# Kernel tuning notes

Measured on AMD Instinct MI355X. Metric: run time of the kernel, lower is better.

## Reference

```python
import jax, jax.numpy as jnp
import numpy as np

# db4 analysis filters (pywt convention); synthesis reuses same filters (orthogonal wavelet,
# correlation analysis + convolution synthesis gives perfect reconstruction under periodization).
DEC_LO = [-0.010597401784997278, 0.032883011666982945, 0.030841381835986965, -0.18703481171888114,
          -0.02798376941698385, 0.6308807679295904, 0.7148465705525415, 0.23037781330885523]
DEC_HI = [-0.23037781330885523, 0.7148465705525415, -0.6308807679295904, -0.02798376941698385,
          0.18703481171888114, 0.030841381835986965, -0.032883011666982945, -0.010597401784997278]
LEVELS = 3

def _analysis(x, filt):
    # a[n] = sum_k filt[k] * x[(2n+k) mod L]  (circular filter + downsample-by-2)
    y = sum(c * jnp.roll(x, -k, axis=-1) for k, c in enumerate(filt))
    return y[..., ::2]

def _synthesis(a, filt):
    # upsample-by-2 (zeros at odd positions) then circular convolution with filt
    u = jnp.zeros(a.shape[:-1] + (2 * a.shape[-1],), a.dtype).at[..., ::2].set(a)
    return sum(c * jnp.roll(u, k, axis=-1) for k, c in enumerate(filt))

def _decompose(z, levels):
    details, cur = [], z
    for _ in range(levels):
        details.append(_analysis(cur, DEC_HI))
        cur = _analysis(cur, DEC_LO)
    return cur, details

def _reconstruct(approx, details):
    cur = approx
    for d in reversed(details):
        cur = _synthesis(cur, DEC_LO) + _synthesis(d, DEC_HI)
    return cur

def _soft_threshold(c, lam_raw):
    # dynamic per-(batch,channel) threshold scaled by learnable softplus(lam_raw)
    lam = jax.nn.softplus(lam_raw) * jnp.mean(jnp.abs(c), axis=-1)  # [B,H]
    thr = jnp.sign(c) * jnp.maximum(jnp.abs(c) - lam[..., None], 0.0)
    return thr, lam

def _film(c, flow_raw, Wgb, bgb, Wg, bg):
    # FiLM gamma/beta from flow features, sigmoid-gated
    gb = flow_raw @ Wgb.T + bgb                      # [B, 2H]
    H = c.shape[1]
    gamma, beta = gb[:, :H], gb[:, H:]
    gate = jax.nn.sigmoid(flow_raw @ Wg + bg)[:, None, None]  # [B,1,1]
    return c * (1.0 + gate * gamma[:, :, None]) + gate * beta[:, :, None]

def setup_inputs() -> dict:
    key = jax.random.key(0)
    ks = jax.random.split(key, 8)
    B, L, C, Hd = 16, 4096, 64, 128
    x = jax.random.normal(ks[0], (B, L, C), jnp.float32)
    mask = jnp.ones((B, L), jnp.float32)
    flow_raw = jax.random.normal(ks[1], (B, 24), jnp.float32)
    W_in = jax.random.normal(ks[2], (Hd, C), jnp.float32) / np.sqrt(C)
    b_in = jnp.zeros((Hd,), jnp.float32)
    W_mix = jax.random.normal(ks[3], (Hd, Hd), jnp.float32) / np.sqrt(Hd)
    b_mix = jnp.zeros((Hd,), jnp.float32)
    lam_raw = jnp.full((LEVELS + 1,), 0.5413248538970947, jnp.float32)  # softplus^-1(1.0)
    film_Wgb = jax.random.normal(ks[4], (LEVELS + 1, 2 * Hd, 24), jnp.float32) * 0.05
    film_bgb = jnp.zeros((LEVELS + 1, 2 * Hd), jnp.float32)
    film_Wg = jax.random.normal(ks[5], (LEVELS + 1, 24), jnp.float32) * 0.05
    film_bg = jnp.zeros((LEVELS + 1,), jnp.float32)
    return dict(x=x, mask=mask, flow_raw=flow_raw, W_in=W_in, b_in=b_in, W_mix=W_mix, b_mix=b_mix,
                lam_raw=lam_raw, film_Wgb=film_Wgb, film_bgb=film_bgb, film_Wg=film_Wg, film_bg=film_bg)

def reference(x, mask, flow_raw, W_in, b_in, W_mix, b_mix, lam_raw, film_Wgb, film_bgb, film_Wg, film_bg):
    xp = x.transpose(0, 2, 1) * mask[:, None, :]               # [B,C,L]
    z = jnp.einsum('hc,bcl->bhl', W_in, xp) + b_in[:, None]    # input_proj (1x1 conv)
    approx, details = _decompose(z, LEVELS)
    approx = _film(approx, flow_raw, film_Wgb[0], film_bgb[0], film_Wg[0], film_bg[0])
    details = [_film(d, flow_raw, film_Wgb[i + 1], film_bgb[i + 1], film_Wg[i + 1], film_bg[i + 1])
               for i, d in enumerate(details)]
    approx_t, lam_a = _soft_threshold(approx, lam_raw[0])
    dts, lams = [], [lam_a]
    for i, d in enumerate(details):
        dt, lam_d = _soft_threshold(d, lam_raw[i + 1])
        dts.append(dt)
        lams.append(lam_d)
    z_rec = _reconstruct(approx_t, dts)
    mixed = jnp.einsum('gh,bhl->bgl', W_mix, z + z_rec) + b_mix[:, None]  # mix (1x1 conv)
    out = jax.nn.gelu(mixed, approximate=False)                 # torch nn.GELU is exact
    h_seq = out.transpose(0, 2, 1) * mask[..., None]            # [B,L,H]
    denom = jnp.clip(jnp.sum(mask, axis=1, keepdims=True), 1.0, None)
    h_pool = jnp.sum(h_seq * mask[..., None], axis=1) / denom   # masked mean pool [B,H]
    lam_cat = jnp.concatenate([l.reshape(l.shape[0], -1) for l in lams], axis=1)
    return h_seq, h_pool, jnp.mean(lam_cat, axis=1), jnp.max(lam_cat, axis=1)
```

## Files before the change

kernel.cpp:

```cpp
#include <hip/hip_runtime.h>
#include <math.h>

#define BB 16
#define LL 4096
#define CC 64
#define HD 128

typedef __attribute__((ext_vector_type(8))) short short8;
typedef __attribute__((ext_vector_type(8))) unsigned short ushort8;
typedef __attribute__((ext_vector_type(4))) float floatx4;

__constant__ float c_lo[8] = {
    -0.010597401784997278f, 0.032883011666982945f, 0.030841381835986965f,
    -0.18703481171888114f, -0.02798376941698385f, 0.6308807679295904f,
    0.7148465705525415f, 0.23037781330885523f};
__constant__ float c_hi[8] = {
    -0.23037781330885523f, 0.7148465705525415f, -0.6308807679295904f,
    -0.02798376941698385f, 0.18703481171888114f, 0.030841381835986965f,
    -0.032883011666982945f, -0.010597401784997278f};

__device__ __forceinline__ float gelu_fast(float x) {
    float u = x * fmaf(0.044715f * x, x, 1.0f) * 1.5957691216057308f;
    return x / (1.0f + __expf(-u));
}
__device__ __forceinline__ unsigned short f2b(float f) {
    unsigned int u = __float_as_uint(f);
    u = u + 0x7FFFu + ((u >> 16) & 1u);
    return (unsigned short)(u >> 16);
}
__device__ __forceinline__ float b2f(unsigned short s) {
    return __uint_as_float(((unsigned int)s) << 16);
}


__global__ __launch_bounds__(256) void zproj_kernel(
    const float* __restrict__ x, const float* __restrict__ mask,
    const float* __restrict__ W_in, const float* __restrict__ b_in,
    unsigned short* __restrict__ z_bf,
    const float* __restrict__ W_mix, unsigned short* __restrict__ Bmix,
    const float* __restrict__ flow, const float* __restrict__ Wgb,
    const float* __restrict__ bgb, const float* __restrict__ Wg,
    const float* __restrict__ bg, float* __restrict__ film_ws,
    float* __restrict__ gate_ws) {
    int blk = blockIdx.x;
    int tid = threadIdx.x;

    if (blk >= BB * 64) {
        int e = blk - BB * 64;
        if (e < 64) {
            int q = e * 256 + tid;
            int g = (q >> 3) & 127;
            int h = ((q >> 10) << 3) | (q & 7);
            Bmix[q] = f2b(W_mix[g * HD + h]);
        } else {
            int bf = e - 64;
            int f = bf & 3;
            int b = bf >> 2;
            const float* fl = flow + b * 24;
            const float* wrow = Wgb + ((size_t)(f * 256 + tid)) * 24;
            float acc = bgb[f * 256 + tid];
#pragma unroll
            for (int j = 0; j < 24; ++j) acc = fmaf(wrow[j], fl[j], acc);
            film_ws[(size_t)bf * 256 + tid] = acc;
            if (tid == 0) {
                float g = bg[f];
#pragma unroll
                for (int j = 0; j < 24; ++j) g = fmaf(Wg[f * 24 + j], fl[j], g);
                gate_ws[bf] = 1.0f / (1.0f + expf(-g));
            }
        }
        return;
    }

    int b = blk >> 6;
    int l0 = (blk & 63) << 6;
    int lane = tid & 63;
    int w = tid >> 6;
    int h_half = w >> 1;
    int l_q = w & 1;
    int ln15 = lane & 15, lq4 = lane >> 4;

    int lr0 = l0 + l_q * 32 + ln15;
    int lr1 = lr0 + 16;
    float mk0 = mask[(size_t)b * LL + lr0];
    float mk1 = mask[(size_t)b * LL + lr1];

    floatx4 acc[4][2];
#pragma unroll
    for (int i = 0; i < 4; ++i)
#pragma unroll
        for (int j = 0; j < 2; ++j) acc[i][j] = (floatx4){0.f, 0.f, 0.f, 0.f};

#pragma unroll
    for (int ks = 0; ks < 2; ++ks) {
        int c0 = ks * 32 + (lq4 << 3);
        short8 bf0, bf1;
        {
            const float* xp = x + ((size_t)b * LL + lr0) * CC + c0;
            float4 xa = *(const float4*)xp;
            float4 xb = *(const float4*)(xp + 4);
            bf0[0] = (short)f2b(xa.x * mk0); bf0[1] = (short)f2b(xa.y * mk0);
            bf0[2] = (short)f2b(xa.z * mk0); bf0[3] = (short)f2b(xa.w * mk0);
            bf0[4] = (short)f2b(xb.x * mk0); bf0[5] = (short)f2b(xb.y * mk0);
            bf0[6] = (short)f2b(xb.z * mk0); bf0[7] = (short)f2b(xb.w * mk0);
        }
        {
            const float* xp = x + ((size_t)b * LL + lr1) * CC + c0;
            float4 xa = *(const float4*)xp;
            float4 xb = *(const float4*)(xp + 4);
            bf1[0] = (short)f2b(xa.x * mk1); bf1[1] = (short)f2b(xa.y * mk1);
            bf1[2] = (short)f2b(xa.z * mk1); bf1[3] = (short)f2b(xa.w * mk1);
            bf1[4] = (short)f2b(xb.x * mk1); bf1[5] = (short)f2b(xb.y * mk1);
            bf1[6] = (short)f2b(xb.z * mk1); bf1[7] = (short)f2b(xb.w * mk1);
        }
        const float* wb = W_in + (size_t)(h_half * 64 + ln15) * CC + c0;
#pragma unroll
        for (int ht = 0; ht < 4; ++ht) {
            const float* wr = wb + (size_t)ht * 16 * CC;
            float4 wa = *(const float4*)wr;
            float4 wc = *(const float4*)(wr + 4);
            short8 af;
            af[0] = (short)f2b(wa.x); af[1] = (short)f2b(wa.y);
            af[2] = (short)f2b(wa.z); af[3] = (short)f2b(wa.w);
            af[4] = (short)f2b(wc.x); af[5] = (short)f2b(wc.y);
            af[6] = (short)f2b(wc.z); af[7] = (short)f2b(wc.w);
            acc[ht][0] = __builtin_amdgcn_mfma_f32_16x16x32_bf16(bf0, af, acc[ht][0], 0, 0, 0);
            acc[ht][1] = __builtin_amdgcn_mfma_f32_16x16x32_bf16(bf1, af, acc[ht][1], 0, 0, 0);
        }
    }

#pragma unroll
    for (int ht = 0; ht < 4; ++ht) {
        int h = h_half * 64 + ht * 16 + ln15;
        float bi = b_in[h];
        unsigned short* zr = z_bf + ((size_t)(b * HD + h)) * LL;
#pragma unroll
        for (int j = 0; j < 2; ++j) {
            int lbase = l0 + l_q * 32 + j * 16 + (lq4 << 2);
            ushort4 o;
            o.x = f2b(acc[ht][j][0] + bi);
            o.y = f2b(acc[ht][j][1] + bi);
            o.z = f2b(acc[ht][j][2] + bi);
            o.w = f2b(acc[ht][j][3] + bi);
            *(ushort4*)(zr + lbase) = o;
        }
    }
}


__device__ __forceinline__ void analysis_step(const float* __restrict__ src,
                                              float* __restrict__ lo_dst,
                                              float* __restrict__ hi_dst,
                                              int half, int tid) {
    int len = half << 1;
    for (int q = tid; q < (half >> 2); q += 256) {
        int n0 = q << 2;
        float lo[4], hi[4];
        if (n0 + 4 == half) {
#pragma unroll
            for (int i = 0; i < 4; ++i) {
                float l = 0.f, hh = 0.f;
#pragma unroll
                for (int k = 0; k < 8; ++k) {
                    float v = src[(2 * (n0 + i) + k) & (len - 1)];
                    l = fmaf(c_lo[k], v, l);
                    hh = fmaf(c_hi[k], v, hh);
                }
                lo[i] = l; hi[i] = hh;
            }
        } else {
            float sv[16];
            const float* sp = src + (n0 << 1);
            *(float4*)&sv[0]  = *(const float4*)(sp);
            *(float4*)&sv[4]  = *(const float4*)(sp + 4);
            *(float4*)&sv[8]  = *(const float4*)(sp + 8);
            *(float4*)&sv[12] = *(const float4*)(sp + 12);
#pragma unroll
            for (int i = 0; i < 4; ++i) {
                float l = 0.f, hh = 0.f;
#pragma unroll
                for (int k = 0; k < 8; ++k) {
                    l = fmaf(c_lo[k], sv[2 * i + k], l);
                    hh = fmaf(c_hi[k], sv[2 * i + k], hh);
                }
                lo[i] = l; hi[i] = hh;
            }
        }
        *(float4*)&lo_dst[n0] = make_float4(lo[0], lo[1], lo[2], lo[3]);
        *(float4*)&hi_dst[n0] = make_float4(hi[0], hi[1], hi[2], hi[3]);
    }
}

__device__ __forceinline__ void synth_oct(const float* __restrict__ A,
                                          const float* __restrict__ D,
                                          int m0, int half, float* ov) {
    if (m0 == 0) {
        int mask2 = (half << 1) - 1;
#pragma unroll
        for (int t = 0; t < 8; ++t) {
            int par = t & 1;
            float s = 0.f;
#pragma unroll
            for (int j = 0; j < 4; ++j) {
                int k = 2 * j + par;
                int idx = ((t - k) & mask2) >> 1;
                s = fmaf(c_lo[k], A[idx], s);
                s = fmaf(c_hi[k], D[idx], s);
            }
            ov[t] = s;
        }
    } else {
        float av[8], dv[8];
        *(float4*)&av[0] = *(const float4*)(A + m0 - 4);
        *(float4*)&av[4] = *(const float4*)(A + m0);
        *(float4*)&dv[0] = *(const float4*)(D + m0 - 4);
        *(float4*)&dv[4] = *(const float4*)(D + m0);
#pragma unroll
        for (int t = 0; t < 4; ++t) {
            float e = 0.f, o = 0.f;
#pragma unroll
            for (int j = 0; j < 4; ++j) {
                float xa = av[t + 4 - j], xd = dv[t + 4 - j];
                e = fmaf(c_lo[2 * j], xa, e);     e = fmaf(c_hi[2 * j], xd, e);
                o = fmaf(c_lo[2 * j + 1], xa, o); o = fmaf(c_hi[2 * j + 1], xd, o);
            }
            ov[2 * t] = e;
            ov[2 * t + 1] = o;
        }
    }
}

__device__ __forceinline__ void synth_step(const float* __restrict__ A,
                                           const float* __restrict__ D,
                                           float* __restrict__ dst,
                                           int half, int tid) {
    for (int q = tid; q < (half >> 2); q += 256) {
        int m0 = q << 2;
        int i0 = m0 << 1;
        float ov[8];
        synth_oct(A, D, m0, half, ov);
        *(float4*)&dst[i0]     = make_float4(ov[0], ov[1], ov[2], ov[3]);
        *(float4*)&dst[i0 + 4] = make_float4(ov[4], ov[5], ov[6], ov[7]);
    }
}


__global__ __launch_bounds__(256) void wavelet_kernel(const unsigned short* __restrict__ z_bf,
                                                      unsigned short* __restrict__ s_bf,
                                                      const float* __restrict__ film_ws,
                                                      const float* __restrict__ gate_ws,
                                                      const float* __restrict__ lam_raw,
                                                      float* __restrict__ lam_ws) {
    __shared__ float d1[2048];
    __shared__ float d2[1024];
    __shared__ float Aq[2048];
    __shared__ float Bq[1024];

    int blk = blockIdx.x;
    int b = blk >> 7;
    int h = blk & 127;
    int tid = threadIdx.x;
    const unsigned short* zg = z_bf + ((size_t)(b * HD + h)) * LL;
    unsigned short* sg = s_bf + ((size_t)(b * HD + h)) * LL;

    for (int q = tid; q < 512; q += 256) {
        int n0 = q << 2;
        float sv[16];
        if (n0 == 2044) {
#pragma unroll
            for (int j = 0; j < 14; ++j)
                sv[j] = b2f(zg[(2 * n0 + j) & 4095]);
            sv[14] = 0.f; sv[15] = 0.f;
        } else {
            ushort8 va = *(const ushort8*)(zg + (n0 << 1));
            ushort8 vb = *(const ushort8*)(zg + (n0 << 1) + 8);
#pragma unroll
            for (int j = 0; j < 8; ++j) {
                sv[j]     = b2f(va[j]);
                sv[8 + j] = b2f(vb[j]);
            }
        }
        float lo[4], hi[4];
#pragma unroll
        for (int i = 0; i < 4; ++i) {
            float l = 0.f, hh = 0.f;
#pragma unroll
            for (int k = 0; k < 8; ++k) {
                l = fmaf(c_lo[k], sv[2 * i + k], l);
                hh = fmaf(c_hi[k], sv[2 * i + k], hh);
            }
            lo[i] = l; hi[i] = hh;
        }
        *(float4*)&Aq[n0] = make_float4(lo[0], lo[1], lo[2], lo[3]);
        *(float4*)&d1[n0] = make_float4(hi[0], hi[1], hi[2], hi[3]);
    }
    __syncthreads();
    analysis_step(Aq, Bq, d2, 1024, tid);
    __syncthreads();
    analysis_step(Bq, Aq, Aq + 512, 512, tid);
    __syncthreads();

    float sc0, sh0, sc1, sh1, sc2, sh2, sc3, sh3;
    {
        int base = b * 4;
#define FILM_COEF(bd, SC, SH)                                              \
        {   float ga = film_ws[((size_t)(base + bd)) * 256 + h];           \
            float be = film_ws[((size_t)(base + bd)) * 256 + 128 + h];     \
            float gt = gate_ws[base + bd];                                 \
            SC = 1.0f + gt * ga; SH = gt * be; }
        FILM_COEF(0, sc0, sh0) FILM_COEF(1, sc1, sh1)
        FILM_COEF(2, sc2, sh2) FILM_COEF(3, sc3, sh3)
#undef FILM_COEF
    }

    float* p0 = &Aq[tid << 2];
    float* p1 = &d1[tid << 2];
    float* p2 = &d1[1024 + (tid << 2)];
    float* p3 = &d2[tid << 2];
    bool lowhalf = (tid < 128);
    float scA = lowhalf ? sc0 : sc3, shA = lowhalf ? sh0 : sh3;

    float4 f0 = *(float4*)p0, f1 = *(float4*)p1, f2v = *(float4*)p2, f3 = *(float4*)p3;
#define FILMV(V, SC, SH)                                                   \
    { V.x = fmaf(V.x, SC, SH); V.y = fmaf(V.y, SC, SH);                    \
      V.z = fmaf(V.z, SC, SH); V.w = fmaf(V.w, SC, SH); }
    FILMV(f0, scA, shA) FILMV(f1, sc1, sh1) FILMV(f2v, sc1, sh1) FILMV(f3, sc2, sh2)
#undef FILMV
    float sA = fabsf(f0.x) + fabsf(f0.y) + fabsf(f0.z) + fabsf(f0.w);
    float s1 = fabsf(f1.x) + fabsf(f1.y) + fabsf(f1.z) + fabsf(f1.w)
             + fabsf(f2v.x) + fabsf(f2v.y) + fabsf(f2v.z) + fabsf(f2v.w);
    float s2 = fabsf(f3.x) + fabsf(f3.y) + fabsf(f3.z) + fabsf(f3.w);
#pragma unroll
    for (int off = 32; off > 0; off >>= 1) {
        sA += __shfl_xor(sA, off);
        s1 += __shfl_xor(s1, off);
        s2 += __shfl_xor(s2, off);
    }
    if ((tid & 63) == 0)
        ((float4*)Bq)[tid >> 6] = make_float4(lowhalf ? sA : 0.f, s1, s2,
                                              lowhalf ? 0.f : sA);
    __syncthreads();
    float4 r0 = ((const float4*)Bq)[0];
    float4 r1 = ((const float4*)Bq)[1];
    float4 r2 = ((const float4*)Bq)[2];
    float4 r3 = ((const float4*)Bq)[3];
    float lam0 = log1pf(expf(lam_raw[0])) * ((r0.x + r1.x + r2.x + r3.x) * (1.0f / 512.f));
    float lam1 = log1pf(expf(lam_raw[1])) * ((r0.y + r1.y + r2.y + r3.y) * (1.0f / 2048.f));
    float lam2 = log1pf(expf(lam_raw[2])) * ((r0.z + r1.z + r2.z + r3.z) * (1.0f / 1024.f));
    float lam3 = log1pf(expf(lam_raw[3])) * ((r0.w + r1.w + r2.w + r3.w) * (1.0f / 512.f));
    if (tid < 4) {
        float lam = (tid == 0) ? lam0 : (tid == 1) ? lam1 : (tid == 2) ? lam2 : lam3;
        lam_ws[((size_t)(b * 4 + tid)) * 128 + h] = lam;
    }
    float lamA = lowhalf ? lam0 : lam3;
#define THRV(V, LAM)                                                       \
    { float a;                                                             \
      a = fabsf(V.x) - (LAM); V.x = (a > 0.f) ? copysignf(a, V.x) : 0.f;   \
      a = fabsf(V.y) - (LAM); V.y = (a > 0.f) ? copysignf(a, V.y) : 0.f;   \
      a = fabsf(V.z) - (LAM); V.z = (a > 0.f) ? copysignf(a, V.z) : 0.f;   \
      a = fabsf(V.w) - (LAM); V.w = (a > 0.f) ? copysignf(a, V.w) : 0.f; }
    THRV(f0, lamA) THRV(f1, lam1) THRV(f2v, lam1) THRV(f3, lam2)
#undef THRV
    *(float4*)p0 = f0; *(float4*)p1 = f1; *(float4*)p2 = f2v; *(float4*)p3 = f3;
    __syncthreads();

    synth_step(Aq, Aq + 512, Bq, 512, tid);
    __syncthreads();
    synth_step(Bq, d2, Aq, 1024, tid);
    __syncthreads();
    for (int q = tid; q < 512; q += 256) {
        int m0 = q << 2;
        int i0 = m0 << 1;
        float ov[8];
        synth_oct(Aq, d1, m0, 2048, ov);
        ushort8 zin = *(const ushort8*)(zg + i0);
        ushort8 o8;
#pragma unroll
        for (int t = 0; t < 8; ++t) o8[t] = f2b(ov[t] + b2f(zin[t]));
        *(ushort8*)(sg + i0) = o8;
    }
}


union U32x4S8 { unsigned int u[4]; short8 s; };

__global__ __launch_bounds__(256) void mix_kernel(const unsigned short* __restrict__ s_bf,
                                                  const unsigned short* __restrict__ Bmix,
                                                  const float* __restrict__ b_mix,
                                                  const float* __restrict__ mask,
                                                  float* __restrict__ out,
                                                  float* __restrict__ pool_part) {
    __shared__ unsigned int T[HD * 32];
    __shared__ float pbuf[2][HD];

    int blk = blockIdx.x;
    int b = blk >> 6;
    int lt64 = blk & 63;
    int l0 = lt64 << 6;
    int tid = threadIdx.x;
    int lane = tid & 63;
    int w = tid >> 6;
    int l_half = w >> 1, g_half = w & 1;
    int ln15 = lane & 15, lq4 = lane >> 4;

    {
        const unsigned int* src = (const unsigned int*)s_bf;
#pragma unroll
        for (int r = 0; r < 4; ++r) {
            int q = (r << 8) + tid;
            int hh = q >> 3;
            int k = q & 7;
            uint4 v = *(const uint4*)(src + (size_t)(b * HD + hh) * (LL / 2) +
                                      (l0 >> 1) + (k << 2));
            int sw = hh & 31;
            unsigned int* tp = T + hh * 32;
            tp[((k << 2) + 0) ^ sw] = v.x;
            tp[((k << 2) + 1) ^ sw] = v.y;
            tp[((k << 2) + 2) ^ sw] = v.z;
            tp[((k << 2) + 3) ^ sw] = v.w;
        }
    }
    __syncthreads();

    floatx4 acc[2][4];
#pragma unroll
    for (int i = 0; i < 2; ++i)
#pragma unroll
        for (int j = 0; j < 4; ++j) acc[i][j] = (floatx4){0.f, 0.f, 0.f, 0.f};

    const unsigned short* Bb = Bmix + (g_half * 64 + ln15) * 8;

#pragma unroll 2
    for (int ks = 0; ks < 4; ++ks) {
        int koct = ks * 4 + lq4;
        short8 a[2], bb[4];
#pragma unroll
        for (int lt = 0; lt < 2; ++lt) {
            int l_loc = l_half * 32 + lt * 16 + ln15;
            int lp = l_loc >> 1;
            int odd = l_loc & 1;
            U32x4S8 cv;
#pragma unroll
            for (int qq = 0; qq < 4; ++qq) {
                int h0 = koct * 8 + 2 * qq;
                unsigned int w0 = T[h0 * 32 + (lp ^ (h0 & 31))];
                unsigned int w1 = T[(h0 + 1) * 32 + (lp ^ ((h0 + 1) & 31))];
                unsigned int e0 = odd ? (w0 >> 16) : (w0 & 0xffffu);
                unsigned int e1 = odd ? (w1 >> 16) : (w1 & 0xffffu);
                cv.u[qq] = e0 | (e1 << 16);
            }
            a[lt] = cv.s;
        }
#pragma unroll
        for (int gt = 0; gt < 4; ++gt)
            bb[gt] = *(const short8*)(Bb + (size_t)koct * 1024 + gt * 128);
#pragma unroll
        for (int lt = 0; lt < 2; ++lt)
#pragma unroll
            for (int gt = 0; gt < 4; ++gt)
                acc[lt][gt] = __builtin_amdgcn_mfma_f32_16x16x32_bf16(bb[gt], a[lt], acc[lt][gt], 0, 0, 0);
    }

    float4 pacc4[4];
#pragma unroll
    for (int gt = 0; gt < 4; ++gt) pacc4[gt] = make_float4(0.f, 0.f, 0.f, 0.f);

#pragma unroll
    for (int lt = 0; lt < 2; ++lt) {
        int l = l0 + l_half * 32 + lt * 16 + ln15;
        float mkv = mask[(size_t)b * LL + l];
        float* orow = out + ((size_t)b * LL + l) * HD;
#pragma unroll
        for (int gt = 0; gt < 4; ++gt) {
            int g0q = g_half * 64 + gt * 16 + (lq4 << 2);
            float4 bm = *(const float4*)&b_mix[g0q];
            float4 v;
            v.x = gelu_fast(acc[lt][gt][0] + bm.x) * mkv;
            v.y = gelu_fast(acc[lt][gt][1] + bm.y) * mkv;
            v.z = gelu_fast(acc[lt][gt][2] + bm.z) * mkv;
            v.w = gelu_fast(acc[lt][gt][3] + bm.w) * mkv;
            *(float4*)&orow[g0q] = v;
            pacc4[gt].x = fmaf(v.x, mkv, pacc4[gt].x);
            pacc4[gt].y = fmaf(v.y, mkv, pacc4[gt].y);
            pacc4[gt].z = fmaf(v.z, mkv, pacc4[gt].z);
            pacc4[gt].w = fmaf(v.w, mkv, pacc4[gt].w);
        }
    }
#pragma unroll
    for (int gt = 0; gt < 4; ++gt) {
#pragma unroll
        for (int off = 1; off <= 8; off <<= 1) {
            pacc4[gt].x += __shfl_xor(pacc4[gt].x, off);
            pacc4[gt].y += __shfl_xor(pacc4[gt].y, off);
            pacc4[gt].z += __shfl_xor(pacc4[gt].z, off);
            pacc4[gt].w += __shfl_xor(pacc4[gt].w, off);
        }
    }
    if (ln15 == 0) {
#pragma unroll
        for (int gt = 0; gt < 4; ++gt)
            *(float4*)&pbuf[l_half][g_half * 64 + gt * 16 + (lq4 << 2)] = pacc4[gt];
    }
    __syncthreads();
    if (tid < HD)
        pool_part[((size_t)(b * 64 + lt64)) * HD + tid] = pbuf[0][tid] + pbuf[1][tid];
}


__global__ void finalize_kernel(const float* __restrict__ pool_part,
                                const float* __restrict__ mask,
                                const float* __restrict__ lam_ws,
                                float* __restrict__ d_out) {
    const size_t OUT1 = (size_t)BB * LL * HD;
    const size_t OUT2 = OUT1 + (size_t)BB * HD;
    const size_t OUT3 = OUT2 + BB;
    int b = blockIdx.x, tid = threadIdx.x;
    __shared__ float rsum[256], rmax[256];
    __shared__ float dsh;

    float ms = 0.f;
    const float4* mp = (const float4*)(mask + (size_t)b * LL);
    for (int i = tid; i < LL / 4; i += 256) {
        float4 m = mp[i];
        ms += m.x + m.y + m.z + m.w;
    }
    rsum[tid] = ms; __syncthreads();
    for (int st = 128; st > 0; st >>= 1) {
        if (tid < st) rsum[tid] += rsum[tid + st];
        __syncthreads();
    }
    if (tid == 0) dsh = fmaxf(rsum[0], 1.0f);
    __syncthreads();
    float denom = dsh;
    __syncthreads();

    {
        int hh = tid & 127, half = tid >> 7;
        float s = 0.f;
        for (int blk = half * 32; blk < half * 32 + 32; ++blk)
            s += pool_part[((size_t)(b * 64 + blk)) * HD + hh];
        rsum[tid] = s;
        __syncthreads();
        if (tid < 128)
            d_out[OUT1 + (size_t)b * HD + tid] = (rsum[tid] + rsum[tid + 128]) / denom;
        __syncthreads();
    }

    float v0 = lam_ws[(size_t)b * 512 + tid];
    float v1 = lam_ws[(size_t)b * 512 + 256 + tid];
    rsum[tid] = v0 + v1;
    rmax[tid] = fmaxf(v0, v1);
    __syncthreads();
    for (int st = 128; st > 0; st >>= 1) {
        if (tid < st) {
            rsum[tid] += rsum[tid + st];
            rmax[tid] = fmaxf(rmax[tid], rmax[tid + st]);
        }
        __syncthreads();
    }
    if (tid == 0) {
        d_out[OUT2 + b] = rsum[0] / 512.0f;
        d_out[OUT3 + b] = rmax[0];
    }
}


extern "C" void kernel_launch(void* const* d_in, const int* in_sizes, int n_in,
                              void* d_out, int out_size, void* d_ws, size_t ws_size,
                              hipStream_t stream) {
    (void)in_sizes; (void)n_in; (void)out_size; (void)ws_size;
    const float* x      = (const float*)d_in[0];
    const float* mask   = (const float*)d_in[1];
    const float* flow   = (const float*)d_in[2];
    const float* W_in   = (const float*)d_in[3];
    const float* b_in   = (const float*)d_in[4];
    const float* W_mix  = (const float*)d_in[5];
    const float* b_mix  = (const float*)d_in[6];
    const float* lam_raw= (const float*)d_in[7];
    const float* Wgb    = (const float*)d_in[8];
    const float* bgb    = (const float*)d_in[9];
    const float* Wg     = (const float*)d_in[10];
    const float* bg     = (const float*)d_in[11];

    unsigned short* z_bf = (unsigned short*)d_ws;
    unsigned short* s_bf = z_bf + (size_t)BB * HD * LL;
    float* film_ws   = (float*)(s_bf + (size_t)BB * HD * LL);
    float* gate_ws   = film_ws + BB * 4 * 256;
    float* lam_ws    = gate_ws + 64;
    float* pool_part = lam_ws + BB * 4 * 128;
    unsigned short* Bmix = (unsigned short*)(pool_part + BB * 64 * HD);

    float* out = (float*)d_out;

    hipLaunchKernelGGL(zproj_kernel, dim3(BB * 64 + 128), dim3(256), 0, stream,
                       x, mask, W_in, b_in, z_bf,
                       W_mix, Bmix, flow, Wgb, bgb, Wg, bg, film_ws, gate_ws);
    hipLaunchKernelGGL(wavelet_kernel, dim3(BB * HD), dim3(256), 0, stream,
                       z_bf, s_bf, film_ws, gate_ws, lam_raw, lam_ws);
    hipLaunchKernelGGL(mix_kernel, dim3(BB * (LL / 64)), dim3(256), 0, stream,
                       s_bf, Bmix, b_mix, mask, out, pool_part);
    hipLaunchKernelGGL(finalize_kernel, dim3(BB), dim3(256), 0, stream,
                       pool_part, mask, lam_ws, out);
}
```

Measured before the change: 66.67 us.

## Fuse finalize into mix kernel via last-block atomic counter; nontemporal output stores

```diff
diff --git a/kernel.cpp b/kernel.cpp
--- a/kernel.cpp
+++ b/kernel.cpp
@@ -41,7 +41,9 @@
     const float* __restrict__ flow, const float* __restrict__ Wgb,
     const float* __restrict__ bgb, const float* __restrict__ Wg,
     const float* __restrict__ bg, float* __restrict__ film_ws,
-    float* __restrict__ gate_ws) {
+    float* __restrict__ gate_ws, float* __restrict__ denom_ws,
+    unsigned int* __restrict__ cnt) {
+    __shared__ float red[256];
     int blk = blockIdx.x;
     int tid = threadIdx.x;
 
@@ -52,7 +54,7 @@
             int g = (q >> 3) & 127;
             int h = ((q >> 10) << 3) | (q & 7);
             Bmix[q] = f2b(W_mix[g * HD + h]);
-        } else {
+        } else if (e < 128) {
             int bf = e - 64;
             int f = bf & 3;
             int b = bf >> 2;
@@ -67,6 +69,23 @@
 #pragma unroll
                 for (int j = 0; j < 24; ++j) g = fmaf(Wg[f * 24 + j], fl[j], g);
                 gate_ws[bf] = 1.0f / (1.0f + expf(-g));
+            }
+        } else {
+            int b = e - 128;
+            float s = 0.f;
+            const float4* mp = (const float4*)(mask + (size_t)b * LL);
+            for (int i = tid; i < LL / 4; i += 256) {
+                float4 m = mp[i];
+                s += m.x + m.y + m.z + m.w;
+            }
+            red[tid] = s; __syncthreads();
+            for (int st = 128; st > 0; st >>= 1) {
+                if (tid < st) red[tid] += red[tid + st];
+                __syncthreads();
+            }
+            if (tid == 0) {
+                denom_ws[b] = fmaxf(red[0], 1.0f);
+                cnt[b] = 0u;
             }
         }
         return;
@@ -388,10 +407,14 @@
                                                   const unsigned short* __restrict__ Bmix,
                                                   const float* __restrict__ b_mix,
                                                   const float* __restrict__ mask,
-                                                  float* __restrict__ out,
-                                                  float* __restrict__ pool_part) {
+                                                  float* __restrict__ dout,
+                                                  float* __restrict__ pool_part,
+                                                  const float* __restrict__ lam_ws,
+                                                  const float* __restrict__ denom_ws,
+                                                  unsigned int* __restrict__ cnt) {
     __shared__ unsigned int T[HD * 32];
     __shared__ float pbuf[2][HD];
+    __shared__ int lastFlag;
 
     int blk = blockIdx.x;
     int b = blk >> 6;
@@ -469,21 +492,21 @@
     for (int lt = 0; lt < 2; ++lt) {
         int l = l0 + l_half * 32 + lt * 16 + ln15;
         float mkv = mask[(size_t)b * LL + l];
-        float* orow = out + ((size_t)b * LL + l) * HD;
+        float* orow = dout + ((size_t)b * LL + l) * HD;
 #pragma unroll
         for (int gt = 0; gt < 4; ++gt) {
             int g0q = g_half * 64 + gt * 16 + (lq4 << 2);
             float4 bm = *(const float4*)&b_mix[g0q];
-            float4 v;
-            v.x = gelu_fast(acc[lt][gt][0] + bm.x) * mkv;
-            v.y = gelu_fast(acc[lt][gt][1] + bm.y) * mkv;
-            v.z = gelu_fast(acc[lt][gt][2] + bm.z) * mkv;
-            v.w = gelu_fast(acc[lt][gt][3] + bm.w) * mkv;
-            *(float4*)&orow[g0q] = v;
-            pacc4[gt].x = fmaf(v.x, mkv, pacc4[gt].x);
-            pacc4[gt].y = fmaf(v.y, mkv, pacc4[gt].y);
-            pacc4[gt].z = fmaf(v.z, mkv, pacc4[gt].z);
-            pacc4[gt].w = fmaf(v.w, mkv, pacc4[gt].w);
+            floatx4 v;
+            v[0] = gelu_fast(acc[lt][gt][0] + bm.x) * mkv;
+            v[1] = gelu_fast(acc[lt][gt][1] + bm.y) * mkv;
+            v[2] = gelu_fast(acc[lt][gt][2] + bm.z) * mkv;
+            v[3] = gelu_fast(acc[lt][gt][3] + bm.w) * mkv;
+            __builtin_nontemporal_store(v, (floatx4*)&orow[g0q]);
+            pacc4[gt].x = fmaf(v[0], mkv, pacc4[gt].x);
+            pacc4[gt].y = fmaf(v[1], mkv, pacc4[gt].y);
+            pacc4[gt].z = fmaf(v[2], mkv, pacc4[gt].z);
+            pacc4[gt].w = fmaf(v[3], mkv, pacc4[gt].w);
         }
     }
 #pragma unroll
@@ -504,63 +527,50 @@
     __syncthreads();
     if (tid < HD)
         pool_part[((size_t)(b * 64 + lt64)) * HD + tid] = pbuf[0][tid] + pbuf[1][tid];
-}
-
-
-__global__ void finalize_kernel(const float* __restrict__ pool_part,
-                                const float* __restrict__ mask,
-                                const float* __restrict__ lam_ws,
-                                float* __restrict__ d_out) {
+
+    __threadfence();
+    if (tid == 0) {
+        unsigned int old = atomicAdd(&cnt[b], 1u);
+        lastFlag = (old == 63u);
+    }
+    __syncthreads();
+    if (!lastFlag) return;
+    __threadfence();
+
     const size_t OUT1 = (size_t)BB * LL * HD;
     const size_t OUT2 = OUT1 + (size_t)BB * HD;
     const size_t OUT3 = OUT2 + BB;
-    int b = blockIdx.x, tid = threadIdx.x;
-    __shared__ float rsum[256], rmax[256];
-    __shared__ float dsh;
-
-    float ms = 0.f;
-    const float4* mp = (const float4*)(mask + (size_t)b * LL);
-    for (int i = tid; i < LL / 4; i += 256) {
-        float4 m = mp[i];
-        ms += m.x + m.y + m.z + m.w;
-    }
-    rsum[tid] = ms; __syncthreads();
-    for (int st = 128; st > 0; st >>= 1) {
-        if (tid < st) rsum[tid] += rsum[tid + st];
-        __syncthreads();
-    }
-    if (tid == 0) dsh = fmaxf(rsum[0], 1.0f);
-    __syncthreads();
-    float denom = dsh;
-    __syncthreads();
+    float* red = (float*)T;
+    float* rmx = red + 256;
+    float denom = denom_ws[b];
 
     {
-        int hh = tid & 127, half = tid >> 7;
+        int hh = tid & 127, half2 = tid >> 7;
         float s = 0.f;
-        for (int blk = half * 32; blk < half * 32 + 32; ++blk)
-            s += pool_part[((size_t)(b * 64 + blk)) * HD + hh];
-        rsum[tid] = s;
+        for (int blk2 = half2 * 32; blk2 < half2 * 32 + 32; ++blk2)
+            s += pool_part[((size_t)(b * 64 + blk2)) * HD + hh];
+        red[tid] = s;
         __syncthreads();
         if (tid < 128)
-            d_out[OUT1 + (size_t)b * HD + tid] = (rsum[tid] + rsum[tid + 128]) / denom;
+            dout[OUT1 + (size_t)b * HD + tid] = (red[tid] + red[tid + 128]) / denom;
         __syncthreads();
     }
 
     float v0 = lam_ws[(size_t)b * 512 + tid];
     float v1 = lam_ws[(size_t)b * 512 + 256 + tid];
-    rsum[tid] = v0 + v1;
-    rmax[tid] = fmaxf(v0, v1);
+    red[tid] = v0 + v1;
+    rmx[tid] = fmaxf(v0, v1);
     __syncthreads();
     for (int st = 128; st > 0; st >>= 1) {
         if (tid < st) {
-            rsum[tid] += rsum[tid + st];
-            rmax[tid] = fmaxf(rmax[tid], rmax[tid + st]);
+            red[tid] += red[tid + st];
+            rmx[tid] = fmaxf(rmx[tid], rmx[tid + st]);
         }
         __syncthreads();
     }
     if (tid == 0) {
-        d_out[OUT2 + b] = rsum[0] / 512.0f;
-        d_out[OUT3 + b] = rmax[0];
+        dout[OUT2 + b] = red[0] / 512.0f;
+        dout[OUT3 + b] = rmx[0];
     }
 }
 
@@ -588,17 +598,18 @@
     float* gate_ws   = film_ws + BB * 4 * 256;
     float* lam_ws    = gate_ws + 64;
     float* pool_part = lam_ws + BB * 4 * 128;
-    unsigned short* Bmix = (unsigned short*)(pool_part + BB * 64 * HD);
+    float* denom_ws  = pool_part + (size_t)BB * 64 * HD;
+    unsigned int* cnt = (unsigned int*)(denom_ws + 16);
+    unsigned short* Bmix = (unsigned short*)(cnt + 16);
 
     float* out = (float*)d_out;
 
-    hipLaunchKernelGGL(zproj_kernel, dim3(BB * 64 + 128), dim3(256), 0, stream,
+    hipLaunchKernelGGL(zproj_kernel, dim3(BB * 64 + 144), dim3(256), 0, stream,
                        x, mask, W_in, b_in, z_bf,
-                       W_mix, Bmix, flow, Wgb, bgb, Wg, bg, film_ws, gate_ws);
+                       W_mix, Bmix, flow, Wgb, bgb, Wg, bg, film_ws, gate_ws,
+                       denom_ws, cnt);
     hipLaunchKernelGGL(wavelet_kernel, dim3(BB * HD), dim3(256), 0, stream,
                        z_bf, s_bf, film_ws, gate_ws, lam_raw, lam_ws);
     hipLaunchKernelGGL(mix_kernel, dim3(BB * (LL / 64)), dim3(256), 0, stream,
-                       s_bf, Bmix, b_mix, mask, out, pool_part);
-    hipLaunchKernelGGL(finalize_kernel, dim3(BB), dim3(256), 0, stream,
-                       pool_part, mask, lam_ws, out);
-}
+                       s_bf, Bmix, b_mix, mask, out, pool_part, lam_ws, denom_ws, cnt);
+}
```

Measured after the change: 186.7 us. 180% more time.

## Stage bf16 W_in in LDS and pair-interleave transpose tile for wider LDS reads

Applied to the files above, without the earlier changes.

```diff
diff --git a/kernel.cpp b/kernel.cpp
--- a/kernel.cpp
+++ b/kernel.cpp
@@ -42,6 +42,7 @@
     const float* __restrict__ bgb, const float* __restrict__ Wg,
     const float* __restrict__ bg, float* __restrict__ film_ws,
     float* __restrict__ gate_ws) {
+    __shared__ unsigned short Wl[HD * CC];
     int blk = blockIdx.x;
     int tid = threadIdx.x;
 
@@ -72,6 +73,21 @@
         return;
     }
 
+#pragma unroll
+    for (int j = 0; j < 4; ++j) {
+        int ci = (tid << 2) + j;
+        int h = ci >> 3, cc = ci & 7;
+        const float* wr = W_in + (size_t)h * CC + (cc << 3);
+        float4 wa = *(const float4*)wr;
+        float4 wb = *(const float4*)(wr + 4);
+        short8 sf;
+        sf[0] = (short)f2b(wa.x); sf[1] = (short)f2b(wa.y);
+        sf[2] = (short)f2b(wa.z); sf[3] = (short)f2b(wa.w);
+        sf[4] = (short)f2b(wb.x); sf[5] = (short)f2b(wb.y);
+        sf[6] = (short)f2b(wb.z); sf[7] = (short)f2b(wb.w);
+        *(short8*)&Wl[(((h << 3) + (cc ^ (h & 7))) << 3)] = sf;
+    }
+
     int b = blk >> 6;
     int l0 = (blk & 63) << 6;
     int lane = tid & 63;
@@ -79,6 +95,7 @@
     int h_half = w >> 1;
     int l_q = w & 1;
     int ln15 = lane & 15, lq4 = lane >> 4;
+    int hp = ln15 & 7;
 
     int lr0 = l0 + l_q * 32 + ln15;
     int lr1 = lr0 + 16;
@@ -90,6 +107,8 @@
     for (int i = 0; i < 4; ++i)
 #pragma unroll
         for (int j = 0; j < 2; ++j) acc[i][j] = (floatx4){0.f, 0.f, 0.f, 0.f};
+
+    __syncthreads();
 
 #pragma unroll
     for (int ks = 0; ks < 2; ++ks) {
@@ -113,17 +132,11 @@
             bf1[4] = (short)f2b(xb.x * mk1); bf1[5] = (short)f2b(xb.y * mk1);
             bf1[6] = (short)f2b(xb.z * mk1); bf1[7] = (short)f2b(xb.w * mk1);
         }
-        const float* wb = W_in + (size_t)(h_half * 64 + ln15) * CC + c0;
+        int cc = (ks << 2) + lq4;
 #pragma unroll
         for (int ht = 0; ht < 4; ++ht) {
-            const float* wr = wb + (size_t)ht * 16 * CC;
-            float4 wa = *(const float4*)wr;
-            float4 wc = *(const float4*)(wr + 4);
-            short8 af;
-            af[0] = (short)f2b(wa.x); af[1] = (short)f2b(wa.y);
-            af[2] = (short)f2b(wa.z); af[3] = (short)f2b(wa.w);
-            af[4] = (short)f2b(wc.x); af[5] = (short)f2b(wc.y);
-            af[6] = (short)f2b(wc.z); af[7] = (short)f2b(wc.w);
+            int hrow = h_half * 64 + ht * 16 + ln15;
+            short8 af = *(const short8*)&Wl[(((hrow << 3) + (cc ^ hp)) << 3)];
             acc[ht][0] = __builtin_amdgcn_mfma_f32_16x16x32_bf16(bf0, af, acc[ht][0], 0, 0, 0);
             acc[ht][1] = __builtin_amdgcn_mfma_f32_16x16x32_bf16(bf1, af, acc[ht][1], 0, 0, 0);
         }
@@ -412,12 +425,12 @@
             int k = q & 7;
             uint4 v = *(const uint4*)(src + (size_t)(b * HD + hh) * (LL / 2) +
                                       (l0 >> 1) + (k << 2));
-            int sw = hh & 31;
-            unsigned int* tp = T + hh * 32;
-            tp[((k << 2) + 0) ^ sw] = v.x;
-            tp[((k << 2) + 1) ^ sw] = v.y;
-            tp[((k << 2) + 2) ^ sw] = v.z;
-            tp[((k << 2) + 3) ^ sw] = v.w;
+            int h2 = hh >> 1, par = hh & 1, sw = h2 & 31;
+            unsigned int* tp = T + (h2 << 6);
+            tp[((((k << 2) + 0) ^ sw) << 1) + par] = v.x;
+            tp[((((k << 2) + 1) ^ sw) << 1) + par] = v.y;
+            tp[((((k << 2) + 2) ^ sw) << 1) + par] = v.z;
+            tp[((((k << 2) + 3) ^ sw) << 1) + par] = v.w;
         }
     }
     __syncthreads();
@@ -442,11 +455,11 @@
             U32x4S8 cv;
 #pragma unroll
             for (int qq = 0; qq < 4; ++qq) {
-                int h0 = koct * 8 + 2 * qq;
-                unsigned int w0 = T[h0 * 32 + (lp ^ (h0 & 31))];
-                unsigned int w1 = T[(h0 + 1) * 32 + (lp ^ ((h0 + 1) & 31))];
-                unsigned int e0 = odd ? (w0 >> 16) : (w0 & 0xffffu);
-                unsigned int e1 = odd ? (w1 >> 16) : (w1 & 0xffffu);
+                int h2 = (koct << 2) + qq;
+                int sw = h2 & 31;
+                uint2 w01 = *(const uint2*)&T[(h2 << 6) + ((lp ^ sw) << 1)];
+                unsigned int e0 = odd ? (w01.x >> 16) : (w01.x & 0xffffu);
+                unsigned int e1 = odd ? (w01.y >> 16) : (w01.y & 0xffffu);
                 cv.u[qq] = e0 | (e1 << 16);
             }
             a[lt] = cv.s;
```

After: 64.75 us (median of 2 runs). 1.03x faster.
